# Kernel optimization log

Measured on AMD Instinct MI355X. Metric: run time of the kernel, lower is better.

The kernel has to match this reference:

```python
import jax, jax.numpy as jnp
import numpy as np

B, N, D, V, LAYERS = 2, 1024, 64, 6, 2


def setup_inputs() -> dict:
    key = jax.random.key(0)
    ks = jax.random.split(key, 20)
    s = lambda k, shp, fan: jax.random.normal(k, shp, jnp.float32) / np.sqrt(fan)
    return {
        'input_data': jax.random.randint(ks[0], (B, N), 0, V),
        'coordinate': jax.random.normal(ks[1], (B, N, 3), jnp.float32),
        'mask': jnp.ones((B, N), dtype=bool),
        'emb': s(ks[2], (V, D), 1.0),
        'We1': s(ks[3], (2 * D + 1, D), 2 * D + 1), 'be1': jnp.zeros((D,), jnp.float32),
        'We2': s(ks[4], (D, D), D), 'be2': jnp.zeros((D,), jnp.float32),
        'Wx1': s(ks[5], (D, D), D), 'bx1': jnp.zeros((D,), jnp.float32),
        'Wx2': s(ks[6], (D, 1), D), 'bx2': jnp.zeros((1,), jnp.float32),
        'Wh1': s(ks[7], (D, D), D), 'bh1': jnp.zeros((D,), jnp.float32),
        'Wh2': s(ks[8], (D, D), D), 'bh2': jnp.zeros((D,), jnp.float32),
        'Winf': s(ks[9], (D, 1), D), 'binf': jnp.zeros((1,), jnp.float32),
        'Wout': s(ks[10], (D, 1), D), 'bout': jnp.zeros((1,), jnp.float32),
    }


def reference(input_data, coordinate, mask, emb, We1, be1, We2, be2,
              Wx1, bx1, Wx2, bx2, Wh1, bh1, Wh2, bh2, Winf, binf, Wout, bout):
    H = emb[input_data]                          # (b,N,d)
    m = mask.astype(coordinate.dtype)            # (b,N)
    me = m[:, :, None]                           # (b,N,1)
    msq = (m[:, :, None] * m[:, None, :])[..., None]  # (b,N,N,1)
    X = coordinate
    d = H.shape[-1]
    Wa, Wb, wc = We1[:d], We1[d:2 * d], We1[2 * d:]    # split concat weight
    for _ in range(LAYERS):
        diff = X[:, :, None, :] - X[:, None, :, :]      # (b,N,N,3)
        x12 = jnp.sum(diff * diff * msq, -1, keepdims=True)  # (b,N,N,1)
        # phi_e(cat[H1,H2,x12]) without materializing the concat
        pre = (jnp.einsum('bik,kd->bid', H, Wa)[:, :, None, :]
               + jnp.einsum('bjk,kd->bjd', H, Wb)[:, None, :, :]
               + x12 @ wc + be1)                        # (b,N,N,d)
        M = jnp.tanh(jnp.tanh(pre) @ We2 + be2) * msq   # (b,N,N,d)
        E = jax.nn.sigmoid(M @ Winf + binf)             # (b,N,N,1)
        M2 = jnp.sum(M * E, axis=1)                     # (b,N,d)
        phiX = jnp.tanh(jnp.tanh(M @ Wx1 + bx1) @ Wx2 + bx2)  # (b,N,N,1)
        X = X + jnp.sum(diff * msq * phiX, axis=1)      # (b,N,3)
        H = (jnp.tanh(jnp.tanh(M2 @ Wh1 + bh1) @ Wh2 + bh2) + H) * me
    Hm = jnp.mean(H * me, axis=-2)                      # (b,d)
    return jax.nn.relu(Hm) @ Wout + bout                # (b,1)
```

## Files before the change

### kernel.cpp

```cpp
#include <hip/hip_runtime.h>

#define NN 1024
#define DD 64
#define K2F 2.8853900817779268f
#define NL2E 1.4426950408889634f

typedef __attribute__((ext_vector_type(8))) short bh8;
typedef __attribute__((ext_vector_type(4))) float f4;
typedef __attribute__((ext_vector_type(4))) int   i4;

#define MFMA __builtin_amdgcn_mfma_f32_16x16x32_bf16

static __device__ __forceinline__ bh8 asb8(i4 v){ return __builtin_bit_cast(bh8, v); }

#if __has_builtin(__builtin_amdgcn_exp2f)
static __device__ __forceinline__ float fexp2(float x){ return __builtin_amdgcn_exp2f(x); }
#else
extern "C" __device__ float __ocml_exp2_f32(float);
static __device__ __forceinline__ float fexp2(float x){ return __ocml_exp2_f32(x); }
#endif
static __device__ __forceinline__ float frcp(float x){ return __builtin_amdgcn_rcpf(x); }

static __device__ __forceinline__ float tanh_z(float z){
  return fmaf(frcp(1.f + fexp2(z)), -2.f, 1.f);
}
static __device__ __forceinline__ unsigned hibits(float v){ return __float_as_uint(v) & 0xFFFF0000u; }
static __device__ __forceinline__ float hif(float v){ return __uint_as_float(hibits(v)); }
static __device__ __forceinline__ int pack2(float v0, float v1){
  return (int)__builtin_amdgcn_perm(__float_as_uint(v1), __float_as_uint(v0), 0x07060302u);
}

__launch_bounds__(256)
__global__ void prep0_k(const int* __restrict__ ids, const float* __restrict__ emb,
                        const float* __restrict__ We1, const float* __restrict__ be1,
                        float* __restrict__ H0, float* __restrict__ HA, float* __restrict__ HB){
  int wv = threadIdx.x >> 6, ln = threadIdx.x & 63;
  int row = blockIdx.x*4 + wv;
  __shared__ float hl[4][64];
  float h = emb[ids[row]*DD + ln];
  H0[row*DD + ln] = h;
  hl[wv][ln] = h;
  float a = 0.f, bacc = be1[ln];
  #pragma unroll 8
  for (int k = 0; k < DD; ++k){
    float hv = hl[wv][k];
    a    = fmaf(hv, We1[k*DD + ln],      a);
    bacc = fmaf(hv, We1[(DD+k)*DD + ln], bacc);
  }
  HA[row*DD+ln] = K2F*a;
  HB[row*DD+ln] = K2F*bacc;
}

template<bool LAST>
__launch_bounds__(256, 3)
__global__ void pair_k(
    const float* __restrict__ HA,  const float* __restrict__ HB,
    const float* __restrict__ Xin,
    const float* __restrict__ We2, const float* __restrict__ be2,
    const float* __restrict__ Wx1, const float* __restrict__ bx1,
    const float* __restrict__ Wx2, const float* __restrict__ bx2,
    const float* __restrict__ Winf,const float* __restrict__ binf,
    const float* __restrict__ We1,
    float* __restrict__ Ppart)
{
  __shared__ i4 fragW[24][64];
  __shared__ __align__(16) unsigned Mlds[4][1024];
  __shared__ float wcK[64];
  __shared__ float bmK[4][64];
  __shared__ float winfA[64], be2A[64], bx1A[64], wx2A[64];

  const int tid = threadIdx.x;
  const int wv = tid>>6, ln = tid&63;
  const int q = ln>>4, c = ln&15;

  i4* fragHi = (i4*)&Mlds[0][0];
  for (int s = wv; s < 32; s += 4){
    const float* W = (s & 16) ? Wx1 : We2;
    int kh = (s>>2)&1, t = s&3;
    int kbase = kh*32 + q*8, n = t*16 + c;
    int dw[4];
    #pragma unroll
    for (int p = 0; p < 4; ++p){
      float v0 = K2F * W[(kbase+2*p  )*DD + n];
      float v1 = K2F * W[(kbase+2*p+1)*DD + n];
      if (s & 8){ v0 = v0 - hif(v0); v1 = v1 - hif(v1); }
      dw[p] = pack2(v0, v1);
    }
    i4 val = (i4){dw[0],dw[1],dw[2],dw[3]};
    if (s < 8) fragHi[s*64 + ln] = val;
    else       fragW[s-8][ln]   = val;
  }
  if (tid < 64){
    wcK[tid] = K2F * We1[128*DD + tid];
    int tt = tid & 3, m4 = tid >> 2;
    int d = tt*16 + m4;
    winfA[tid] = -NL2E*Winf[d];
    be2A[tid]  = K2F*be2[d];
    bx1A[tid]  = K2F*bx1[d];
    wx2A[tid]  = K2F*Wx2[d];
  }
  __syncthreads();

  i4 whiA[2][4];
  #pragma unroll
  for (int kh=0; kh<2; ++kh)
    #pragma unroll
    for (int t=0; t<4; ++t) whiA[kh][t] = fragHi[(kh*4+t)*64 + ln];
  __syncthreads();

  const float binfs = -NL2E*binf[0];
  const float bx2s  = K2F*bx2[0];

  unsigned* mhi = &Mlds[wv][0];
  unsigned* mlo = &Mlds[wv][512];

  for (int job = 0; job < 2; ++job){
    const int jid = blockIdx.x*2 + job;
    const int jg = jid/3;
    const int third = jid - jg*3;
    const int rowj = jg*4 + wv;
    const int b = rowj >> 10;
    const int ibeg = third ? (third==1 ? 352 : 688) : 0;
    const int iend = ibeg + (third ? 336 : 352);

    bmK[wv][ln] = HB[rowj*DD + ln];
    const float xjx = Xin[rowj*3+0], xjy = Xin[rowj*3+1], xjz = Xin[rowj*3+2];

    float accM2[16];
    #pragma unroll
    for (int u=0;u<16;++u) accM2[u] = 0.f;
    float accX0=0.f, accX1=0.f, accX2=0.f;

    const float* Abase = HA + (size_t)b*NN*DD;
    const float* Xbase = Xin + (size_t)b*NN*3;

    float cxx, cxy, cxz;
    { const float* xp = Xbase + (ibeg+c)*3; cxx = xp[0]; cxy = xp[1]; cxz = xp[2]; }

    for (int i0 = ibeg; i0 < iend; i0 += 16){
      int qz = q, lz = ln;
      asm volatile("" : "+v"(qz), "+v"(lz));

      const float* ap = Abase + (i0+c)*DD + q*8;
      float4 ca0 = *(const float4*)(ap);    float4 ca1 = *(const float4*)(ap+4);
      float4 ca2 = *(const float4*)(ap+32); float4 ca3 = *(const float4*)(ap+36);

      f4 wcA0 = *(const f4*)&wcK[qz*8];      f4 wcA1 = *(const f4*)&wcK[qz*8+4];
      f4 wcA2 = *(const f4*)&wcK[qz*8+32];   f4 wcA3 = *(const f4*)&wcK[qz*8+36];
      const float* bmp = &bmK[wv][0];
      f4 bmA0 = *(const f4*)&bmp[qz*8];      f4 bmA1 = *(const f4*)&bmp[qz*8+4];
      f4 bmA2 = *(const f4*)&bmp[qz*8+32];   f4 bmA3 = *(const f4*)&bmp[qz*8+36];

      float dx = cxx - xjx, dy = cxy - xjy, dz = cxz - xjz;
      float x12 = dx*dx + dy*dy + dz*dz;

      if (i0 + 16 < iend){
        const float* xp = Xbase + (i0+16+c)*3;
        cxx = xp[0]; cxy = xp[1]; cxz = xp[2];
      }

      float av[16] = {ca0.x,ca0.y,ca0.z,ca0.w, ca1.x,ca1.y,ca1.z,ca1.w,
                      ca2.x,ca2.y,ca2.z,ca2.w, ca3.x,ca3.y,ca3.z,ca3.w};
      float wcv[16] = {wcA0[0],wcA0[1],wcA0[2],wcA0[3], wcA1[0],wcA1[1],wcA1[2],wcA1[3],
                       wcA2[0],wcA2[1],wcA2[2],wcA2[3], wcA3[0],wcA3[1],wcA3[2],wcA3[3]};
      float bmv[16] = {bmA0[0],bmA0[1],bmA0[2],bmA0[3], bmA1[0],bmA1[1],bmA1[2],bmA1[3],
                       bmA2[0],bmA2[1],bmA2[2],bmA2[3], bmA3[0],bmA3[1],bmA3[2],bmA3[3]};
      float tv[16];
      #pragma unroll
      for (int u=0; u<16; ++u) tv[u] = tanh_z(fmaf(x12, wcv[u], av[u] + bmv[u]));

      int th0[4], tl0[4], th1[4], tl1[4];
      #pragma unroll
      for (int p=0;p<4;++p){
        float a0v = tv[2*p],   b0v = tv[2*p+1];
        float a1v = tv[8+2*p], b1v = tv[8+2*p+1];
        th0[p] = pack2(a0v,b0v);
        tl0[p] = pack2(a0v-hif(a0v), b0v-hif(b0v));
        th1[p] = pack2(a1v,b1v);
        tl1[p] = pack2(a1v-hif(a1v), b1v-hif(b1v));
      }
      bh8 Th[2] = { asb8((i4){th0[0],th0[1],th0[2],th0[3]}), asb8((i4){th1[0],th1[1],th1[2],th1[3]}) };
      bh8 Tl[2] = { asb8((i4){tl0[0],tl0[1],tl0[2],tl0[3]}), asb8((i4){tl1[0],tl1[1],tl1[2],tl1[3]}) };

      float m[4][4];
      #pragma unroll
      for (int t=0;t<4;++t){
        f4 a = (f4){0.f,0.f,0.f,0.f};
        #pragma unroll
        for (int kh=0;kh<2;++kh){
          i4 wl = fragW[kh*4 + t][lz];
          a = MFMA(asb8(whiA[kh][t]), Th[kh], a, 0,0,0);
          a = MFMA(asb8(whiA[kh][t]), Tl[kh], a, 0,0,0);
          a = MFMA(asb8(wl),          Th[kh], a, 0,0,0);
        }
        f4 beA = *(const f4*)&be2A[qz*16 + t*0 + 0];
        (void)beA;
        #pragma unroll
        for (int r=0;r<4;++r){
          float mv = tanh_z(a[r] + be2A[qz*16 + r*4 + t]);
          m[t][r] = mv;
        }
        if (!LAST){
          unsigned h0 = (unsigned)pack2(m[t][0], m[t][1]);
          unsigned h1 = (unsigned)pack2(m[t][2], m[t][3]);
          unsigned l0 = (unsigned)pack2(m[t][0]-hif(m[t][0]), m[t][1]-hif(m[t][1]));
          unsigned l1 = (unsigned)pack2(m[t][2]-hif(m[t][2]), m[t][3]-hif(m[t][3]));
          int dwa = c*32 + ((2*t + (qz>>1)) ^ (c&7))*4 + (qz&1)*2;
          *(uint2*)&mhi[dwa] = make_uint2(h0,h1);
          *(uint2*)&mlo[dwa] = make_uint2(l0,l1);
        }
      }

      float p = 0.f;
      #pragma unroll
      for (int t=0;t<4;++t)
        #pragma unroll
        for (int r=0;r<4;++r) p = fmaf(m[t][r], winfA[qz*16 + r*4 + t], p);
      p += __shfl_xor(p, 16, 64);
      p += __shfl_xor(p, 32, 64);
      float er = frcp(1.f + fexp2(p + binfs));
      #pragma unroll
      for (int t=0;t<4;++t)
        #pragma unroll
        for (int r=0;r<4;++r) accM2[t*4+r] = fmaf(m[t][r], er, accM2[t*4+r]);

      if (!LAST){
        int ra0 = c*32 + ((0 + qz) ^ (c&7))*4;
        int ra1 = c*32 + ((4 + qz) ^ (c&7))*4;
        i4 bh0 = *(const i4*)&mhi[ra0];
        i4 bh1 = *(const i4*)&mhi[ra1];
        i4 bl0 = *(const i4*)&mlo[ra0];
        i4 bl1 = *(const i4*)&mlo[ra1];

        float pdl = 0.f;
        #pragma unroll
        for (int t=0;t<4;++t){
          f4 g = (f4){0.f,0.f,0.f,0.f};
          {
            i4 wh = fragW[ 8 + t][lz];
            i4 wl = fragW[16 + t][lz];
            g = MFMA(asb8(wh), asb8(bh0), g, 0,0,0);
            g = MFMA(asb8(wh), asb8(bl0), g, 0,0,0);
            g = MFMA(asb8(wl), asb8(bh0), g, 0,0,0);
          }
          {
            i4 wh = fragW[12 + t][lz];
            i4 wl = fragW[20 + t][lz];
            g = MFMA(asb8(wh), asb8(bh1), g, 0,0,0);
            g = MFMA(asb8(wh), asb8(bl1), g, 0,0,0);
            g = MFMA(asb8(wl), asb8(bh1), g, 0,0,0);
          }
          #pragma unroll
          for (int r=0;r<4;++r){
            float th = tanh_z(g[r] + bx1A[qz*16 + r*4 + t]);
            pdl = fmaf(th, wx2A[qz*16 + r*4 + t], pdl);
          }
        }
        pdl += __shfl_xor(pdl, 16, 64);
        pdl += __shfl_xor(pdl, 32, 64);
        float px = tanh_z(pdl + bx2s);
        accX0 = fmaf(dx, px, accX0);
        accX1 = fmaf(dy, px, accX1);
        accX2 = fmaf(dz, px, accX2);
      }
    }

    #pragma unroll
    for (int u=0;u<16;++u){
      accM2[u] += __shfl_xor(accM2[u], 1, 64);
      accM2[u] += __shfl_xor(accM2[u], 2, 64);
      accM2[u] += __shfl_xor(accM2[u], 4, 64);
      accM2[u] += __shfl_xor(accM2[u], 8, 64);
    }
    float* pp = Ppart + ((size_t)rowj*3 + third)*68;
    if (!LAST){
      accX0 += __shfl_xor(accX0,1,64); accX0 += __shfl_xor(accX0,2,64);
      accX0 += __shfl_xor(accX0,4,64); accX0 += __shfl_xor(accX0,8,64);
      accX1 += __shfl_xor(accX1,1,64); accX1 += __shfl_xor(accX1,2,64);
      accX1 += __shfl_xor(accX1,4,64); accX1 += __shfl_xor(accX1,8,64);
      accX2 += __shfl_xor(accX2,1,64); accX2 += __shfl_xor(accX2,2,64);
      accX2 += __shfl_xor(accX2,4,64); accX2 += __shfl_xor(accX2,8,64);
      if (ln == 0){ pp[64] = accX0; pp[65] = accX1; pp[66] = accX2; }
    }
    if (c == 0){
      #pragma unroll
      for (int t=0;t<4;++t)
        #pragma unroll
        for (int r=0;r<4;++r) pp[t*16 + q*4 + r] = accM2[t*4+r];
    }
  }
}

__launch_bounds__(256)
__global__ void finprep_k(const float* __restrict__ Ppart,
                          const float* __restrict__ Xin, const float* __restrict__ Hin,
                          const float* __restrict__ Wh1, const float* __restrict__ bh1,
                          const float* __restrict__ Wh2, const float* __restrict__ bh2,
                          const float* __restrict__ We1, const float* __restrict__ be1,
                          float* __restrict__ Xout, float* __restrict__ Hout,
                          float* __restrict__ HA, float* __restrict__ HB,
                          int do_prep, int do_x){
  __shared__ float m2lds[4][64];
  __shared__ float h1lds[4][64];
  int wv = threadIdx.x>>6, ln = threadIdx.x&63;
  int jg = blockIdx.x*4 + wv;
  const float* p0 = Ppart + (size_t)jg*3*68;
  const float* p1 = p0 + 68;
  const float* p2 = p0 + 136;
  m2lds[wv][ln] = p0[ln] + p1[ln] + p2[ln];
  float a1 = 0.f;
  #pragma unroll 8
  for (int k=0;k<DD;++k) a1 = fmaf(m2lds[wv][k], Wh1[k*DD+ln], a1);
  float h1 = tanh_z(K2F*(a1 + bh1[ln]));
  h1lds[wv][ln] = h1;
  float a2 = 0.f;
  #pragma unroll 8
  for (int k=0;k<DD;++k) a2 = fmaf(h1lds[wv][k], Wh2[k*DD+ln], a2);
  float h2 = tanh_z(K2F*(a2 + bh2[ln])) + Hin[jg*DD+ln];
  Hout[jg*DD+ln] = h2;
  if (do_x && ln < 3) Xout[jg*3+ln] = Xin[jg*3+ln] + p0[64+ln] + p1[64+ln] + p2[64+ln];
  if (do_prep){
    m2lds[wv][ln] = h2;
    float a = 0.f, bacc = be1[ln];
    #pragma unroll 8
    for (int k = 0; k < DD; ++k){
      float hv = m2lds[wv][k];
      a    = fmaf(hv, We1[k*DD + ln],      a);
      bacc = fmaf(hv, We1[(DD+k)*DD + ln], bacc);
    }
    HA[jg*DD+ln] = K2F*a;
    HB[jg*DD+ln] = K2F*bacc;
  }
}

__global__ void final_k(const float* __restrict__ H, const float* __restrict__ Wout,
                        const float* __restrict__ bout, float* __restrict__ out){
  int b = blockIdx.x, tid = threadIdx.x;
  float acc = 0.f;
  for (int n = tid>>6; n < NN; n += 4) acc += H[((size_t)b*NN+n)*DD + (tid&63)];
  __shared__ float red[4][64];
  red[tid>>6][tid&63] = acc;
  __syncthreads();
  if (tid < 64){
    float s = red[0][tid]+red[1][tid]+red[2][tid]+red[3][tid];
    float v = fmaxf(s * (1.f/NN), 0.f) * Wout[tid];
    #pragma unroll
    for (int o = 1; o < 64; o <<= 1) v += __shfl_xor(v, o, 64);
    if (tid == 0) out[b] = v + bout[0];
  }
}

extern "C" void kernel_launch(void* const* d_in, const int* in_sizes, int n_in,
                              void* d_out, int out_size, void* d_ws, size_t ws_size,
                              hipStream_t stream){
  const int*   ids   = (const int*)  d_in[0];
  const float* coord = (const float*)d_in[1];
  const float* emb  = (const float*)d_in[3];
  const float* We1  = (const float*)d_in[4];
  const float* be1  = (const float*)d_in[5];
  const float* We2  = (const float*)d_in[6];
  const float* be2  = (const float*)d_in[7];
  const float* Wx1  = (const float*)d_in[8];
  const float* bx1  = (const float*)d_in[9];
  const float* Wx2  = (const float*)d_in[10];
  const float* bx2  = (const float*)d_in[11];
  const float* Wh1  = (const float*)d_in[12];
  const float* bh1  = (const float*)d_in[13];
  const float* Wh2  = (const float*)d_in[14];
  const float* bh2  = (const float*)d_in[15];
  const float* Winf = (const float*)d_in[16];
  const float* binf = (const float*)d_in[17];
  const float* Wout = (const float*)d_in[18];
  const float* bout = (const float*)d_in[19];

  float* ws = (float*)d_ws;
  float* HA   = ws;
  float* HBm  = ws + 131072;
  float* Hp0  = ws + 262144;
  float* Hp1  = ws + 393216;
  float* Xp0  = ws + 524288;
  float* Xp1  = ws + 530432;
  float* Ppart= ws + 536576;

  prep0_k<<<512,256,0,stream>>>(ids, emb, We1, be1, Hp0, HA, HBm);
  pair_k<false><<<768,256,0,stream>>>(HA, HBm, coord,
                                      We2, be2, Wx1, bx1, Wx2, bx2, Winf, binf, We1,
                                      Ppart);
  finprep_k<<<512,256,0,stream>>>(Ppart, coord, Hp0, Wh1, bh1, Wh2, bh2, We1, be1,
                                  Xp0, Hp1, HA, HBm, 1, 1);
  pair_k<true><<<768,256,0,stream>>>(HA, HBm, Xp0,
                                     We2, be2, Wx1, bx1, Wx2, bx2, Winf, binf, We1,
                                     Ppart);
  finprep_k<<<512,256,0,stream>>>(Ppart, Xp0, Hp1, Wh1, bh1, Wh2, bh2, We1, be1,
                                  Xp1, Hp0, HA, HBm, 0, 0);
  final_k<<<2,256,0,stream>>>(Hp0, Wout, bout, (float*)d_out);
}
```

Baseline: 453.5 us.

## Fuse node update and final reduction into pair kernel via last-block atomics

Removes the finprep and final kernels by having the last of the three blocks finishing each row group (tracked with an atomic counter) do the node MLP update, the X update and the next layer's HA/HB projection. On the last layer, a second per-batch counter lets the final block compute the mean, ReLU and output projection. Counters are zeroed in prep0. This cuts kernel launches and their gaps at the cost of threadfences, atomics and some serialized tail work inside the pair kernel.

```diff
diff --git a/kernel.cpp b/kernel.cpp
--- a/kernel.cpp
+++ b/kernel.cpp
@@ -33,7 +33,14 @@
 __launch_bounds__(256)
 __global__ void prep0_k(const int* __restrict__ ids, const float* __restrict__ emb,
                         const float* __restrict__ We1, const float* __restrict__ be1,
-                        float* __restrict__ H0, float* __restrict__ HA, float* __restrict__ HB){
+                        float* __restrict__ H0, float* __restrict__ HA, float* __restrict__ HB,
+                        unsigned* __restrict__ cnt0, unsigned* __restrict__ cnt1,
+                        unsigned* __restrict__ bcnt){
+  if (threadIdx.x == 0){
+    cnt0[blockIdx.x] = 0u;
+    cnt1[blockIdx.x] = 0u;
+    if (blockIdx.x < 2) bcnt[blockIdx.x] = 0u;
+  }
   int wv = threadIdx.x >> 6, ln = threadIdx.x & 63;
   int row = blockIdx.x*4 + wv;
   __shared__ float hl[4][64];
@@ -60,14 +67,23 @@
     const float* __restrict__ Wx1, const float* __restrict__ bx1,
     const float* __restrict__ Wx2, const float* __restrict__ bx2,
     const float* __restrict__ Winf,const float* __restrict__ binf,
-    const float* __restrict__ We1,
-    float* __restrict__ Ppart)
+    const float* __restrict__ We1, const float* __restrict__ be1,
+    float* __restrict__ Ppart, unsigned* __restrict__ cnt,
+    const float* __restrict__ Hin,
+    const float* __restrict__ Wh1, const float* __restrict__ bh1,
+    const float* __restrict__ Wh2, const float* __restrict__ bh2,
+    float* __restrict__ Xout, float* __restrict__ Hout,
+    float* __restrict__ HAout, float* __restrict__ HBout,
+    float* __restrict__ HsumPart, unsigned* __restrict__ bcnt,
+    const float* __restrict__ Wout, const float* __restrict__ bout,
+    float* __restrict__ outp)
 {
   __shared__ i4 fragW[24][64];
   __shared__ __align__(16) unsigned Mlds[4][1024];
   __shared__ float wcK[64];
   __shared__ float bmK[4][64];
   __shared__ float winfA[64], be2A[64], bx1A[64], wx2A[64];
+  __shared__ int finflag, bflag;
 
   const int tid = threadIdx.x;
   const int wv = tid>>6, ln = tid&63;
@@ -193,8 +209,6 @@
           a = MFMA(asb8(whiA[kh][t]), Tl[kh], a, 0,0,0);
           a = MFMA(asb8(wl),          Th[kh], a, 0,0,0);
         }
-        f4 beA = *(const f4*)&be2A[qz*16 + t*0 + 0];
-        (void)beA;
         #pragma unroll
         for (int r=0;r<4;++r){
           float mv = tanh_z(a[r] + be2A[qz*16 + r*4 + t]);
@@ -288,65 +302,69 @@
         #pragma unroll
         for (int r=0;r<4;++r) pp[t*16 + q*4 + r] = accM2[t*4+r];
     }
-  }
-}
-
-__launch_bounds__(256)
-__global__ void finprep_k(const float* __restrict__ Ppart,
-                          const float* __restrict__ Xin, const float* __restrict__ Hin,
-                          const float* __restrict__ Wh1, const float* __restrict__ bh1,
-                          const float* __restrict__ Wh2, const float* __restrict__ bh2,
-                          const float* __restrict__ We1, const float* __restrict__ be1,
-                          float* __restrict__ Xout, float* __restrict__ Hout,
-                          float* __restrict__ HA, float* __restrict__ HB,
-                          int do_prep, int do_x){
-  __shared__ float m2lds[4][64];
-  __shared__ float h1lds[4][64];
-  int wv = threadIdx.x>>6, ln = threadIdx.x&63;
-  int jg = blockIdx.x*4 + wv;
-  const float* p0 = Ppart + (size_t)jg*3*68;
-  const float* p1 = p0 + 68;
-  const float* p2 = p0 + 136;
-  m2lds[wv][ln] = p0[ln] + p1[ln] + p2[ln];
-  float a1 = 0.f;
-  #pragma unroll 8
-  for (int k=0;k<DD;++k) a1 = fmaf(m2lds[wv][k], Wh1[k*DD+ln], a1);
-  float h1 = tanh_z(K2F*(a1 + bh1[ln]));
-  h1lds[wv][ln] = h1;
-  float a2 = 0.f;
-  #pragma unroll 8
-  for (int k=0;k<DD;++k) a2 = fmaf(h1lds[wv][k], Wh2[k*DD+ln], a2);
-  float h2 = tanh_z(K2F*(a2 + bh2[ln])) + Hin[jg*DD+ln];
-  Hout[jg*DD+ln] = h2;
-  if (do_x && ln < 3) Xout[jg*3+ln] = Xin[jg*3+ln] + p0[64+ln] + p1[64+ln] + p2[64+ln];
-  if (do_prep){
-    m2lds[wv][ln] = h2;
-    float a = 0.f, bacc = be1[ln];
-    #pragma unroll 8
-    for (int k = 0; k < DD; ++k){
-      float hv = m2lds[wv][k];
-      a    = fmaf(hv, We1[k*DD + ln],      a);
-      bacc = fmaf(hv, We1[(DD+k)*DD + ln], bacc);
-    }
-    HA[jg*DD+ln] = K2F*a;
-    HB[jg*DD+ln] = K2F*bacc;
-  }
-}
-
-__global__ void final_k(const float* __restrict__ H, const float* __restrict__ Wout,
-                        const float* __restrict__ bout, float* __restrict__ out){
-  int b = blockIdx.x, tid = threadIdx.x;
-  float acc = 0.f;
-  for (int n = tid>>6; n < NN; n += 4) acc += H[((size_t)b*NN+n)*DD + (tid&63)];
-  __shared__ float red[4][64];
-  red[tid>>6][tid&63] = acc;
-  __syncthreads();
-  if (tid < 64){
-    float s = red[0][tid]+red[1][tid]+red[2][tid]+red[3][tid];
-    float v = fmaxf(s * (1.f/NN), 0.f) * Wout[tid];
-    #pragma unroll
-    for (int o = 1; o < 64; o <<= 1) v += __shfl_xor(v, o, 64);
-    if (tid == 0) out[b] = v + bout[0];
+
+    __threadfence();
+    if (tid == 0){
+      unsigned old = atomicAdd(&cnt[jg], 1u);
+      finflag = (old == 2u);
+    }
+    __syncthreads();
+    if (finflag){
+      __threadfence();
+      const float* p0 = Ppart + (size_t)rowj*3*68;
+      float* scr = (float*)&Mlds[wv][0];
+      scr[ln] = p0[ln] + p0[68+ln] + p0[136+ln];
+      float a1 = 0.f;
+      #pragma unroll 8
+      for (int k=0;k<DD;++k) a1 = fmaf(scr[k], Wh1[k*DD+ln], a1);
+      float h1 = tanh_z(K2F*(a1 + bh1[ln]));
+      scr[64+ln] = h1;
+      float a2 = 0.f;
+      #pragma unroll 8
+      for (int k=0;k<DD;++k) a2 = fmaf(scr[64+k], Wh2[k*DD+ln], a2);
+      float h2 = tanh_z(K2F*(a2 + bh2[ln])) + Hin[rowj*DD+ln];
+      if (!LAST){
+        Hout[rowj*DD+ln] = h2;
+        if (ln < 3) Xout[rowj*3+ln] = Xin[rowj*3+ln] + p0[64+ln] + p0[132+ln] + p0[200+ln];
+        scr[128+ln] = h2;
+        float a = 0.f, bacc = be1[ln];
+        #pragma unroll 8
+        for (int k=0;k<DD;++k){
+          float hv = scr[128+k];
+          a    = fmaf(hv, We1[k*DD + ln],      a);
+          bacc = fmaf(hv, We1[(DD+k)*DD + ln], bacc);
+        }
+        HAout[rowj*DD+ln] = K2F*a;
+        HBout[rowj*DD+ln] = K2F*bacc;
+      } else {
+        bmK[wv][ln] = h2;
+        __syncthreads();
+        if (wv == 0)
+          HsumPart[jg*64 + ln] = bmK[0][ln]+bmK[1][ln]+bmK[2][ln]+bmK[3][ln];
+        __threadfence();
+        if (tid == 0){
+          unsigned ob = atomicAdd(&bcnt[b], 1u);
+          bflag = (ob == 255u);
+        }
+        __syncthreads();
+        if (bflag){
+          __threadfence();
+          float s = 0.f;
+          const float* hp = HsumPart + (size_t)b*256*64;
+          #pragma unroll 8
+          for (int g = wv; g < 256; g += 4) s += hp[g*64 + ln];
+          bmK[wv][ln] = s;
+          __syncthreads();
+          if (wv == 0){
+            float tot = bmK[0][ln]+bmK[1][ln]+bmK[2][ln]+bmK[3][ln];
+            float v = fmaxf(tot*(1.f/NN), 0.f) * Wout[ln];
+            #pragma unroll
+            for (int o = 1; o < 64; o <<= 1) v += __shfl_xor(v, o, 64);
+            if (ln == 0) outp[b] = v + bout[0];
+          }
+        }
+      }
+    }
   }
 }
 
@@ -374,24 +392,28 @@
   const float* bout = (const float*)d_in[19];
 
   float* ws = (float*)d_ws;
-  float* HA   = ws;
-  float* HBm  = ws + 131072;
-  float* Hp0  = ws + 262144;
-  float* Hp1  = ws + 393216;
-  float* Xp0  = ws + 524288;
-  float* Xp1  = ws + 530432;
-  float* Ppart= ws + 536576;
-
-  prep0_k<<<512,256,0,stream>>>(ids, emb, We1, be1, Hp0, HA, HBm);
-  pair_k<false><<<768,256,0,stream>>>(HA, HBm, coord,
-                                      We2, be2, Wx1, bx1, Wx2, bx2, Winf, binf, We1,
-                                      Ppart);
-  finprep_k<<<512,256,0,stream>>>(Ppart, coord, Hp0, Wh1, bh1, Wh2, bh2, We1, be1,
-                                  Xp0, Hp1, HA, HBm, 1, 1);
-  pair_k<true><<<768,256,0,stream>>>(HA, HBm, Xp0,
-                                     We2, be2, Wx1, bx1, Wx2, bx2, Winf, binf, We1,
-                                     Ppart);
-  finprep_k<<<512,256,0,stream>>>(Ppart, Xp0, Hp1, Wh1, bh1, Wh2, bh2, We1, be1,
-                                  Xp1, Hp0, HA, HBm, 0, 0);
-  final_k<<<2,256,0,stream>>>(Hp0, Wout, bout, (float*)d_out);
+  float* HA0  = ws;
+  float* HB0  = ws + 131072;
+  float* HA1  = ws + 262144;
+  float* HB1  = ws + 393216;
+  float* Hp0  = ws + 524288;
+  float* Hp1  = ws + 655360;
+  float* Xp0  = ws + 786432;
+  float* Ppart= ws + 792576;
+  float* Hsum = ws + 1210368;
+  unsigned* cnt0 = (unsigned*)(ws + 1243136);
+  unsigned* cnt1 = cnt0 + 512;
+  unsigned* bcnt = cnt0 + 1024;
+
+  prep0_k<<<512,256,0,stream>>>(ids, emb, We1, be1, Hp0, HA0, HB0, cnt0, cnt1, bcnt);
+  pair_k<false><<<768,256,0,stream>>>(HA0, HB0, coord,
+                                      We2, be2, Wx1, bx1, Wx2, bx2, Winf, binf, We1, be1,
+                                      Ppart, cnt0, Hp0, Wh1, bh1, Wh2, bh2,
+                                      Xp0, Hp1, HA1, HB1,
+                                      Hsum, bcnt, Wout, bout, (float*)d_out);
+  pair_k<true><<<768,256,0,stream>>>(HA1, HB1, Xp0,
+                                     We2, be2, Wx1, bx1, Wx2, bx2, Winf, binf, We1, be1,
+                                     Ppart, cnt1, Hp1, Wh1, bh1, Wh2, bh2,
+                                     Xp0, Hp1, HA1, HB1,
+                                     Hsum, bcnt, Wout, bout, (float*)d_out);
 }
```

Measured after the change: 633.7 us. 1.4x slower.

## Drop low-bf16 split of M in phiX path and re-split pair grid into halves

Applied to the files above, without the earlier changes.

The phiX branch no longer stores or uses the low-order bf16 residual of M, so the Wx1 product uses four MFMAs per tile instead of six and needs half the M staging buffer in LDS. The pair kernel now gives each block one j-row group and one half of the i range, over a larger grid, replacing the two-jobs-per-block thirds split. Occupancy is raised from three to four blocks per CU. Partial sums shrink from three slices to two, and finprep reads them to match. The cost is lower precision in the coordinate update, since M enters Wx1 at plain bf16.

```diff
diff --git a/kernel.cpp b/kernel.cpp
--- a/kernel.cpp
+++ b/kernel.cpp
@@ -2,6 +2,7 @@
 
 #define NN 1024
 #define DD 64
+#define IHALF 512
 #define K2F 2.8853900817779268f
 #define NL2E 1.4426950408889634f
 
@@ -52,7 +53,7 @@
 }
 
 template<bool LAST>
-__launch_bounds__(256, 3)
+__launch_bounds__(256, 4)
 __global__ void pair_k(
     const float* __restrict__ HA,  const float* __restrict__ HB,
     const float* __restrict__ Xin,
@@ -64,7 +65,7 @@
     float* __restrict__ Ppart)
 {
   __shared__ i4 fragW[24][64];
-  __shared__ __align__(16) unsigned Mlds[4][1024];
+  __shared__ __align__(16) unsigned Mlds[4][512];
   __shared__ float wcK[64];
   __shared__ float bmK[4][64];
   __shared__ float winfA[64], be2A[64], bx1A[64], wx2A[64];
@@ -112,182 +113,159 @@
   const float bx2s  = K2F*bx2[0];
 
   unsigned* mhi = &Mlds[wv][0];
-  unsigned* mlo = &Mlds[wv][512];
-
-  for (int job = 0; job < 2; ++job){
-    const int jid = blockIdx.x*2 + job;
-    const int jg = jid/3;
-    const int third = jid - jg*3;
-    const int rowj = jg*4 + wv;
-    const int b = rowj >> 10;
-    const int ibeg = third ? (third==1 ? 352 : 688) : 0;
-    const int iend = ibeg + (third ? 336 : 352);
-
-    bmK[wv][ln] = HB[rowj*DD + ln];
-    const float xjx = Xin[rowj*3+0], xjy = Xin[rowj*3+1], xjz = Xin[rowj*3+2];
-
-    float accM2[16];
-    #pragma unroll
-    for (int u=0;u<16;++u) accM2[u] = 0.f;
-    float accX0=0.f, accX1=0.f, accX2=0.f;
-
-    const float* Abase = HA + (size_t)b*NN*DD;
-    const float* Xbase = Xin + (size_t)b*NN*3;
-
-    float cxx, cxy, cxz;
-    { const float* xp = Xbase + (ibeg+c)*3; cxx = xp[0]; cxy = xp[1]; cxz = xp[2]; }
-
-    for (int i0 = ibeg; i0 < iend; i0 += 16){
-      int qz = q, lz = ln;
-      asm volatile("" : "+v"(qz), "+v"(lz));
-
-      const float* ap = Abase + (i0+c)*DD + q*8;
-      float4 ca0 = *(const float4*)(ap);    float4 ca1 = *(const float4*)(ap+4);
-      float4 ca2 = *(const float4*)(ap+32); float4 ca3 = *(const float4*)(ap+36);
-
-      f4 wcA0 = *(const f4*)&wcK[qz*8];      f4 wcA1 = *(const f4*)&wcK[qz*8+4];
-      f4 wcA2 = *(const f4*)&wcK[qz*8+32];   f4 wcA3 = *(const f4*)&wcK[qz*8+36];
-      const float* bmp = &bmK[wv][0];
-      f4 bmA0 = *(const f4*)&bmp[qz*8];      f4 bmA1 = *(const f4*)&bmp[qz*8+4];
-      f4 bmA2 = *(const f4*)&bmp[qz*8+32];   f4 bmA3 = *(const f4*)&bmp[qz*8+36];
-
-      float dx = cxx - xjx, dy = cxy - xjy, dz = cxz - xjz;
-      float x12 = dx*dx + dy*dy + dz*dz;
-
-      if (i0 + 16 < iend){
-        const float* xp = Xbase + (i0+16+c)*3;
-        cxx = xp[0]; cxy = xp[1]; cxz = xp[2];
+
+  const int half = blockIdx.x & 1;
+  const int rowj = (blockIdx.x>>1)*4 + wv;
+  const int b = rowj >> 10;
+  const int ibeg = half*IHALF, iend = ibeg + IHALF;
+
+  bmK[wv][ln] = HB[rowj*DD + ln];
+  const float xjx = Xin[rowj*3+0], xjy = Xin[rowj*3+1], xjz = Xin[rowj*3+2];
+
+  float accM2[16];
+  #pragma unroll
+  for (int u=0;u<16;++u) accM2[u] = 0.f;
+  float accX0=0.f, accX1=0.f, accX2=0.f;
+
+  const float* Abase = HA + (size_t)b*NN*DD;
+  const float* Xbase = Xin + (size_t)b*NN*3;
+
+  float cxx, cxy, cxz;
+  { const float* xp = Xbase + (ibeg+c)*3; cxx = xp[0]; cxy = xp[1]; cxz = xp[2]; }
+
+  for (int i0 = ibeg; i0 < iend; i0 += 16){
+    int qz = q, lz = ln;
+    asm volatile("" : "+v"(qz), "+v"(lz));
+
+    const float* ap = Abase + (i0+c)*DD + q*8;
+    float4 ca0 = *(const float4*)(ap);    float4 ca1 = *(const float4*)(ap+4);
+    float4 ca2 = *(const float4*)(ap+32); float4 ca3 = *(const float4*)(ap+36);
+
+    f4 wcA0 = *(const f4*)&wcK[qz*8];      f4 wcA1 = *(const f4*)&wcK[qz*8+4];
+    f4 wcA2 = *(const f4*)&wcK[qz*8+32];   f4 wcA3 = *(const f4*)&wcK[qz*8+36];
+    const float* bmp = &bmK[wv][0];
+    f4 bmA0 = *(const f4*)&bmp[qz*8];      f4 bmA1 = *(const f4*)&bmp[qz*8+4];
+    f4 bmA2 = *(const f4*)&bmp[qz*8+32];   f4 bmA3 = *(const f4*)&bmp[qz*8+36];
+
+    float dx = cxx - xjx, dy = cxy - xjy, dz = cxz - xjz;
+    float x12 = dx*dx + dy*dy + dz*dz;
+
+    if (i0 + 16 < iend){
+      const float* xp = Xbase + (i0+16+c)*3;
+      cxx = xp[0]; cxy = xp[1]; cxz = xp[2];
+    }
+
+    float av[16] = {ca0.x,ca0.y,ca0.z,ca0.w, ca1.x,ca1.y,ca1.z,ca1.w,
+                    ca2.x,ca2.y,ca2.z,ca2.w, ca3.x,ca3.y,ca3.z,ca3.w};
+    float wcv[16] = {wcA0[0],wcA0[1],wcA0[2],wcA0[3], wcA1[0],wcA1[1],wcA1[2],wcA1[3],
+                     wcA2[0],wcA2[1],wcA2[2],wcA2[3], wcA3[0],wcA3[1],wcA3[2],wcA3[3]};
+    float bmv[16] = {bmA0[0],bmA0[1],bmA0[2],bmA0[3], bmA1[0],bmA1[1],bmA1[2],bmA1[3],
+                     bmA2[0],bmA2[1],bmA2[2],bmA2[3], bmA3[0],bmA3[1],bmA3[2],bmA3[3]};
+    float tv[16];
+    #pragma unroll
+    for (int u=0; u<16; ++u) tv[u] = tanh_z(fmaf(x12, wcv[u], av[u] + bmv[u]));
+
+    int th0[4], tl0[4], th1[4], tl1[4];
+    #pragma unroll
+    for (int p=0;p<4;++p){
+      float a0v = tv[2*p],   b0v = tv[2*p+1];
+      float a1v = tv[8+2*p], b1v = tv[8+2*p+1];
+      th0[p] = pack2(a0v,b0v);
+      tl0[p] = pack2(a0v-hif(a0v), b0v-hif(b0v));
+      th1[p] = pack2(a1v,b1v);
+      tl1[p] = pack2(a1v-hif(a1v), b1v-hif(b1v));
+    }
+    bh8 Th[2] = { asb8((i4){th0[0],th0[1],th0[2],th0[3]}), asb8((i4){th1[0],th1[1],th1[2],th1[3]}) };
+    bh8 Tl[2] = { asb8((i4){tl0[0],tl0[1],tl0[2],tl0[3]}), asb8((i4){tl1[0],tl1[1],tl1[2],tl1[3]}) };
+
+    float m[4][4];
+    #pragma unroll
+    for (int t=0;t<4;++t){
+      f4 a = (f4){0.f,0.f,0.f,0.f};
+      #pragma unroll
+      for (int kh=0;kh<2;++kh){
+        i4 wl = fragW[kh*4 + t][lz];
+        a = MFMA(asb8(whiA[kh][t]), Th[kh], a, 0,0,0);
+        a = MFMA(asb8(whiA[kh][t]), Tl[kh], a, 0,0,0);
+        a = MFMA(asb8(wl),          Th[kh], a, 0,0,0);
       }
-
-      float av[16] = {ca0.x,ca0.y,ca0.z,ca0.w, ca1.x,ca1.y,ca1.z,ca1.w,
-                      ca2.x,ca2.y,ca2.z,ca2.w, ca3.x,ca3.y,ca3.z,ca3.w};
-      float wcv[16] = {wcA0[0],wcA0[1],wcA0[2],wcA0[3], wcA1[0],wcA1[1],wcA1[2],wcA1[3],
-                       wcA2[0],wcA2[1],wcA2[2],wcA2[3], wcA3[0],wcA3[1],wcA3[2],wcA3[3]};
-      float bmv[16] = {bmA0[0],bmA0[1],bmA0[2],bmA0[3], bmA1[0],bmA1[1],bmA1[2],bmA1[3],
-                       bmA2[0],bmA2[1],bmA2[2],bmA2[3], bmA3[0],bmA3[1],bmA3[2],bmA3[3]};
-      float tv[16];
-      #pragma unroll
-      for (int u=0; u<16; ++u) tv[u] = tanh_z(fmaf(x12, wcv[u], av[u] + bmv[u]));
-
-      int th0[4], tl0[4], th1[4], tl1[4];
-      #pragma unroll
-      for (int p=0;p<4;++p){
-        float a0v = tv[2*p],   b0v = tv[2*p+1];
-        float a1v = tv[8+2*p], b1v = tv[8+2*p+1];
-        th0[p] = pack2(a0v,b0v);
-        tl0[p] = pack2(a0v-hif(a0v), b0v-hif(b0v));
-        th1[p] = pack2(a1v,b1v);
-        tl1[p] = pack2(a1v-hif(a1v), b1v-hif(b1v));
+      #pragma unroll
+      for (int r=0;r<4;++r){
+        float mv = tanh_z(a[r] + be2A[qz*16 + r*4 + t]);
+        m[t][r] = mv;
       }
-      bh8 Th[2] = { asb8((i4){th0[0],th0[1],th0[2],th0[3]}), asb8((i4){th1[0],th1[1],th1[2],th1[3]}) };
-      bh8 Tl[2] = { asb8((i4){tl0[0],tl0[1],tl0[2],tl0[3]}), asb8((i4){tl1[0],tl1[1],tl1[2],tl1[3]}) };
-
-      float m[4][4];
+      if (!LAST){
+        unsigned h0 = (unsigned)pack2(m[t][0], m[t][1]);
+        unsigned h1 = (unsigned)pack2(m[t][2], m[t][3]);
+        int dwa = c*32 + ((2*t + (qz>>1)) ^ (c&7))*4 + (qz&1)*2;
+        *(uint2*)&mhi[dwa] = make_uint2(h0,h1);
+      }
+    }
+
+    float p = 0.f;
+    #pragma unroll
+    for (int t=0;t<4;++t)
+      #pragma unroll
+      for (int r=0;r<4;++r) p = fmaf(m[t][r], winfA[qz*16 + r*4 + t], p);
+    p += __shfl_xor(p, 16, 64);
+    p += __shfl_xor(p, 32, 64);
+    float er = frcp(1.f + fexp2(p + binfs));
+    #pragma unroll
+    for (int t=0;t<4;++t)
+      #pragma unroll
+      for (int r=0;r<4;++r) accM2[t*4+r] = fmaf(m[t][r], er, accM2[t*4+r]);
+
+    if (!LAST){
+      int ra0 = c*32 + ((0 + qz) ^ (c&7))*4;
+      int ra1 = c*32 + ((4 + qz) ^ (c&7))*4;
+      i4 bh0 = *(const i4*)&mhi[ra0];
+      i4 bh1 = *(const i4*)&mhi[ra1];
+
+      float pdl = 0.f;
       #pragma unroll
       for (int t=0;t<4;++t){
-        f4 a = (f4){0.f,0.f,0.f,0.f};
-        #pragma unroll
-        for (int kh=0;kh<2;++kh){
-          i4 wl = fragW[kh*4 + t][lz];
-          a = MFMA(asb8(whiA[kh][t]), Th[kh], a, 0,0,0);
-          a = MFMA(asb8(whiA[kh][t]), Tl[kh], a, 0,0,0);
-          a = MFMA(asb8(wl),          Th[kh], a, 0,0,0);
-        }
-        f4 beA = *(const f4*)&be2A[qz*16 + t*0 + 0];
-        (void)beA;
+        f4 g = (f4){0.f,0.f,0.f,0.f};
+        g = MFMA(asb8(fragW[ 8 + t][lz]), asb8(bh0), g, 0,0,0);
+        g = MFMA(asb8(fragW[16 + t][lz]), asb8(bh0), g, 0,0,0);
+        g = MFMA(asb8(fragW[12 + t][lz]), asb8(bh1), g, 0,0,0);
+        g = MFMA(asb8(fragW[20 + t][lz]), asb8(bh1), g, 0,0,0);
         #pragma unroll
         for (int r=0;r<4;++r){
-          float mv = tanh_z(a[r] + be2A[qz*16 + r*4 + t]);
-          m[t][r] = mv;
-        }
-        if (!LAST){
-          unsigned h0 = (unsigned)pack2(m[t][0], m[t][1]);
-          unsigned h1 = (unsigned)pack2(m[t][2], m[t][3]);
-          unsigned l0 = (unsigned)pack2(m[t][0]-hif(m[t][0]), m[t][1]-hif(m[t][1]));
-          unsigned l1 = (unsigned)pack2(m[t][2]-hif(m[t][2]), m[t][3]-hif(m[t][3]));
-          int dwa = c*32 + ((2*t + (qz>>1)) ^ (c&7))*4 + (qz&1)*2;
-          *(uint2*)&mhi[dwa] = make_uint2(h0,h1);
-          *(uint2*)&mlo[dwa] = make_uint2(l0,l1);
+          float th = tanh_z(g[r] + bx1A[qz*16 + r*4 + t]);
+          pdl = fmaf(th, wx2A[qz*16 + r*4 + t], pdl);
         }
       }
-
-      float p = 0.f;
-      #pragma unroll
-      for (int t=0;t<4;++t)
-        #pragma unroll
-        for (int r=0;r<4;++r) p = fmaf(m[t][r], winfA[qz*16 + r*4 + t], p);
-      p += __shfl_xor(p, 16, 64);
-      p += __shfl_xor(p, 32, 64);
-      float er = frcp(1.f + fexp2(p + binfs));
-      #pragma unroll
-      for (int t=0;t<4;++t)
-        #pragma unroll
-        for (int r=0;r<4;++r) accM2[t*4+r] = fmaf(m[t][r], er, accM2[t*4+r]);
-
-      if (!LAST){
-        int ra0 = c*32 + ((0 + qz) ^ (c&7))*4;
-        int ra1 = c*32 + ((4 + qz) ^ (c&7))*4;
-        i4 bh0 = *(const i4*)&mhi[ra0];
-        i4 bh1 = *(const i4*)&mhi[ra1];
-        i4 bl0 = *(const i4*)&mlo[ra0];
-        i4 bl1 = *(const i4*)&mlo[ra1];
-
-        float pdl = 0.f;
-        #pragma unroll
-        for (int t=0;t<4;++t){
-          f4 g = (f4){0.f,0.f,0.f,0.f};
-          {
-            i4 wh = fragW[ 8 + t][lz];
-            i4 wl = fragW[16 + t][lz];
-            g = MFMA(asb8(wh), asb8(bh0), g, 0,0,0);
-            g = MFMA(asb8(wh), asb8(bl0), g, 0,0,0);
-            g = MFMA(asb8(wl), asb8(bh0), g, 0,0,0);
-          }
-          {
-            i4 wh = fragW[12 + t][lz];
-            i4 wl = fragW[20 + t][lz];
-            g = MFMA(asb8(wh), asb8(bh1), g, 0,0,0);
-            g = MFMA(asb8(wh), asb8(bl1), g, 0,0,0);
-            g = MFMA(asb8(wl), asb8(bh1), g, 0,0,0);
-          }
-          #pragma unroll
-          for (int r=0;r<4;++r){
-            float th = tanh_z(g[r] + bx1A[qz*16 + r*4 + t]);
-            pdl = fmaf(th, wx2A[qz*16 + r*4 + t], pdl);
-          }
-        }
-        pdl += __shfl_xor(pdl, 16, 64);
-        pdl += __shfl_xor(pdl, 32, 64);
-        float px = tanh_z(pdl + bx2s);
-        accX0 = fmaf(dx, px, accX0);
-        accX1 = fmaf(dy, px, accX1);
-        accX2 = fmaf(dz, px, accX2);
-      }
-    }
-
-    #pragma unroll
-    for (int u=0;u<16;++u){
-      accM2[u] += __shfl_xor(accM2[u], 1, 64);
-      accM2[u] += __shfl_xor(accM2[u], 2, 64);
-      accM2[u] += __shfl_xor(accM2[u], 4, 64);
-      accM2[u] += __shfl_xor(accM2[u], 8, 64);
-    }
-    float* pp = Ppart + ((size_t)rowj*3 + third)*68;
-    if (!LAST){
-      accX0 += __shfl_xor(accX0,1,64); accX0 += __shfl_xor(accX0,2,64);
-      accX0 += __shfl_xor(accX0,4,64); accX0 += __shfl_xor(accX0,8,64);
-      accX1 += __shfl_xor(accX1,1,64); accX1 += __shfl_xor(accX1,2,64);
-      accX1 += __shfl_xor(accX1,4,64); accX1 += __shfl_xor(accX1,8,64);
-      accX2 += __shfl_xor(accX2,1,64); accX2 += __shfl_xor(accX2,2,64);
-      accX2 += __shfl_xor(accX2,4,64); accX2 += __shfl_xor(accX2,8,64);
-      if (ln == 0){ pp[64] = accX0; pp[65] = accX1; pp[66] = accX2; }
-    }
-    if (c == 0){
-      #pragma unroll
-      for (int t=0;t<4;++t)
-        #pragma unroll
-        for (int r=0;r<4;++r) pp[t*16 + q*4 + r] = accM2[t*4+r];
-    }
+      pdl += __shfl_xor(pdl, 16, 64);
+      pdl += __shfl_xor(pdl, 32, 64);
+      float px = tanh_z(pdl + bx2s);
+      accX0 = fmaf(dx, px, accX0);
+      accX1 = fmaf(dy, px, accX1);
+      accX2 = fmaf(dz, px, accX2);
+    }
+  }
+
+  #pragma unroll
+  for (int u=0;u<16;++u){
+    accM2[u] += __shfl_xor(accM2[u], 1, 64);
+    accM2[u] += __shfl_xor(accM2[u], 2, 64);
+    accM2[u] += __shfl_xor(accM2[u], 4, 64);
+    accM2[u] += __shfl_xor(accM2[u], 8, 64);
+  }
+  float* pp = Ppart + ((size_t)rowj*2 + half)*68;
+  if (!LAST){
+    accX0 += __shfl_xor(accX0,1,64); accX0 += __shfl_xor(accX0,2,64);
+    accX0 += __shfl_xor(accX0,4,64); accX0 += __shfl_xor(accX0,8,64);
+    accX1 += __shfl_xor(accX1,1,64); accX1 += __shfl_xor(accX1,2,64);
+    accX1 += __shfl_xor(accX1,4,64); accX1 += __shfl_xor(accX1,8,64);
+    accX2 += __shfl_xor(accX2,1,64); accX2 += __shfl_xor(accX2,2,64);
+    accX2 += __shfl_xor(accX2,4,64); accX2 += __shfl_xor(accX2,8,64);
+    if (ln == 0){ pp[64] = accX0; pp[65] = accX1; pp[66] = accX2; }
+  }
+  if (c == 0){
+    #pragma unroll
+    for (int t=0;t<4;++t)
+      #pragma unroll
+      for (int r=0;r<4;++r) pp[t*16 + q*4 + r] = accM2[t*4+r];
   }
 }
 
@@ -304,10 +282,8 @@
   __shared__ float h1lds[4][64];
   int wv = threadIdx.x>>6, ln = threadIdx.x&63;
   int jg = blockIdx.x*4 + wv;
-  const float* p0 = Ppart + (size_t)jg*3*68;
-  const float* p1 = p0 + 68;
-  const float* p2 = p0 + 136;
-  m2lds[wv][ln] = p0[ln] + p1[ln] + p2[ln];
+  const float* p0 = Ppart + (size_t)jg*2*68;
+  m2lds[wv][ln] = p0[ln] + p0[68+ln];
   float a1 = 0.f;
   #pragma unroll 8
   for (int k=0;k<DD;++k) a1 = fmaf(m2lds[wv][k], Wh1[k*DD+ln], a1);
@@ -318,7 +294,7 @@
   for (int k=0;k<DD;++k) a2 = fmaf(h1lds[wv][k], Wh2[k*DD+ln], a2);
   float h2 = tanh_z(K2F*(a2 + bh2[ln])) + Hin[jg*DD+ln];
   Hout[jg*DD+ln] = h2;
-  if (do_x && ln < 3) Xout[jg*3+ln] = Xin[jg*3+ln] + p0[64+ln] + p1[64+ln] + p2[64+ln];
+  if (do_x && ln < 3) Xout[jg*3+ln] = Xin[jg*3+ln] + p0[64+ln] + p0[132+ln];
   if (do_prep){
     m2lds[wv][ln] = h2;
     float a = 0.f, bacc = be1[ln];
@@ -383,14 +359,14 @@
   float* Ppart= ws + 536576;
 
   prep0_k<<<512,256,0,stream>>>(ids, emb, We1, be1, Hp0, HA, HBm);
-  pair_k<false><<<768,256,0,stream>>>(HA, HBm, coord,
+  pair_k<false><<<1024,256,0,stream>>>(HA, HBm, coord,
+                                       We2, be2, Wx1, bx1, Wx2, bx2, Winf, binf, We1,
+                                       Ppart);
+  finprep_k<<<512,256,0,stream>>>(Ppart, coord, Hp0, Wh1, bh1, Wh2, bh2, We1, be1,
+                                  Xp0, Hp1, HA, HBm, 1, 1);
+  pair_k<true><<<1024,256,0,stream>>>(HA, HBm, Xp0,
                                       We2, be2, Wx1, bx1, Wx2, bx2, Winf, binf, We1,
                                       Ppart);
-  finprep_k<<<512,256,0,stream>>>(Ppart, coord, Hp0, Wh1, bh1, Wh2, bh2, We1, be1,
-                                  Xp0, Hp1, HA, HBm, 1, 1);
-  pair_k<true><<<768,256,0,stream>>>(HA, HBm, Xp0,
-                                     We2, be2, Wx1, bx1, Wx2, bx2, Winf, binf, We1,
-                                     Ppart);
   finprep_k<<<512,256,0,stream>>>(Ppart, Xp0, Hp1, Wh1, bh1, Wh2, bh2, We1, be1,
                                   Xp1, Hp0, HA, HBm, 0, 0);
   final_k<<<2,256,0,stream>>>(Hp0, Wout, bout, (float*)d_out);
```

New measurement: 426.1 us. 6.0% less time.
